# Performance work log

Hardware: AMD Instinct MI355X
Metric: run time of the kernel (lower is better)

The kernel has to match this reference:

```python
import jax, jax.numpy as jnp
import numpy as np

B, L, D, K = 8, 256, 256, 64  # batch, slots, n_input, attn_dimension


def setup_inputs() -> dict:
    key = jax.random.key(0)
    k1, k2, k3 = jax.random.split(key, 3)
    inputs = jax.random.normal(k1, (B, L, D), dtype=jnp.float32)
    # torch.nn.Linear weights are [out_features, in_features]; scale to avoid tanh saturation
    W1 = jax.random.normal(k2, (K, 2 * D), dtype=jnp.float32) * (1.0 / np.sqrt(2 * D))
    W2 = jax.random.normal(k3, (1, K), dtype=jnp.float32) * (1.0 / np.sqrt(K))
    return {"inputs": inputs, "W1": W1, "W2": W2}


def reference(inputs, W1, W2):
    # CONCAT branch of SlotAttention:
    #   score[b,i,j] = W2 @ tanh(W1 @ concat(inputs[b,i], inputs[b,j]))
    # Split W1 into the halves acting on the i-part and j-part of the concat
    # (identical math, avoids materializing the [B,L,L,2D] concat tensor).
    d = inputs.shape[-1]
    W1i, W1j = W1[:, :d], W1[:, d:]
    qi = jnp.einsum('bld,kd->blk', inputs, W1i)          # [B,L,K]
    kj = jnp.einsum('bld,kd->blk', inputs, W1j)          # [B,L,K]
    h = jnp.tanh(qi[:, :, None, :] + kj[:, None, :, :])  # [B,L,L,K]
    scores = jnp.einsum('bijk,k->bij', h, W2[0])         # [B,L,L]
    attn = jax.nn.softmax(scores, axis=2)                # softmax over j
    context = jnp.einsum('bij,bjd->bid', attn, inputs)   # [B,L,D]
    return jnp.concatenate([inputs, context], axis=2)    # [B,L,2D]
```

## Files before the change

### kernel.cpp

```cpp
#include <hip/hip_runtime.h>


#define Bn 8
#define Ln 256
#define Dn 256
#define Kn 64
#define ROWS (Bn*Ln)
#define IPB 4

__global__ __launch_bounds__(128) void proj_kernel(
    const float* __restrict__ X,
    const float* __restrict__ W1,
    float* __restrict__ QK)
{
    __shared__ float Xs[8 * 256];
    const int tid = threadIdx.x;
    const int r0 = blockIdx.x * 8;

    const float4* Xg4 = (const float4*)(X + r0 * Dn);
    float4* Xs4 = (float4*)Xs;
    #pragma unroll
    for (int idx = tid; idx < 512; idx += 128) Xs4[idx] = Xg4[idx];
    __syncthreads();

    const int k = tid & 63, half = tid >> 6;
    const float4* Wrow = (const float4*)(W1 + k * (2 * Dn) + half * Dn);
    float acc[8] = {0, 0, 0, 0, 0, 0, 0, 0};
    #pragma unroll 8
    for (int d4 = 0; d4 < 64; ++d4) {
        float4 w = Wrow[d4];
        #pragma unroll
        for (int r = 0; r < 8; ++r) {
            float4 x = ((const float4*)(Xs + r * Dn))[d4];
            float a = acc[r];
            a = fmaf(w.x, x.x, a);
            a = fmaf(w.y, x.y, a);
            a = fmaf(w.z, x.z, a);
            a = fmaf(w.w, x.w, a);
            acc[r] = a;
        }
    }
    #pragma unroll
    for (int r = 0; r < 8; ++r) {
        float e = __expf(2.0f * acc[r]);
        float t = 1.0f - 2.0f / (e + 1.0f);
        t = fminf(0.99999988f, fmaxf(-0.99999988f, t));
        QK[(r0 + r) * 128 + tid] = t;
    }
}

__global__ __launch_bounds__(256) void attn_kernel(
    const float* __restrict__ X,
    const float* __restrict__ QK,
    const float* __restrict__ W2,
    float* __restrict__ out)
{
    __shared__ float tq_s[IPB * Kn];
    __shared__ float w2_s[Kn];
    __shared__ float S[Ln * IPB];

    const int tid = threadIdx.x;
    const int b  = blockIdx.x / (Ln / IPB);
    const int i0 = (blockIdx.x % (Ln / IPB)) * IPB;

    if (tid < Kn) w2_s[tid] = W2[tid];
    {
        int ii = tid >> 6, kk = tid & 63;
        tq_s[ii * Kn + kk] = QK[(b * Ln + i0 + ii) * 128 + kk];
    }

    float tkr[Kn];
    const float4* kj4 = (const float4*)(QK + (b * Ln + tid) * 128 + 64);
    #pragma unroll
    for (int q = 0; q < 16; ++q) {
        float4 v = kj4[q];
        tkr[q * 4 + 0] = v.x; tkr[q * 4 + 1] = v.y;
        tkr[q * 4 + 2] = v.z; tkr[q * 4 + 3] = v.w;
    }
    __syncthreads();

    float s[IPB] = {0, 0, 0, 0};
    const float4* w4  = (const float4*)w2_s;
    const float4* q4a = (const float4*)(tq_s);
    const float4* q4b = (const float4*)(tq_s + Kn);
    const float4* q4c = (const float4*)(tq_s + 2 * Kn);
    const float4* q4d = (const float4*)(tq_s + 3 * Kn);
    #pragma unroll
    for (int k4 = 0; k4 < 16; ++k4) {
        float4 w  = w4[k4];
        float4 q0 = q4a[k4], q1 = q4b[k4], q2 = q4c[k4], q3 = q4d[k4];
        #pragma unroll
        for (int c = 0; c < 4; ++c) {
            float tk = tkr[k4 * 4 + c];
            float wk = (c == 0) ? w.x : (c == 1) ? w.y : (c == 2) ? w.z : w.w;
            float tq0 = (c == 0) ? q0.x : (c == 1) ? q0.y : (c == 2) ? q0.z : q0.w;
            float tq1 = (c == 0) ? q1.x : (c == 1) ? q1.y : (c == 2) ? q1.z : q1.w;
            float tq2 = (c == 0) ? q2.x : (c == 1) ? q2.y : (c == 2) ? q2.z : q2.w;
            float tq3 = (c == 0) ? q3.x : (c == 1) ? q3.y : (c == 2) ? q3.z : q3.w;
            float n0 = tq0 + tk, d0 = fmaf(tq0, tk, 1.0f);
            float n1 = tq1 + tk, d1 = fmaf(tq1, tk, 1.0f);
            float n2 = tq2 + tk, d2 = fmaf(tq2, tk, 1.0f);
            float n3 = tq3 + tk, d3 = fmaf(tq3, tk, 1.0f);
            s[0] = fmaf(wk, n0 * __builtin_amdgcn_rcpf(d0), s[0]);
            s[1] = fmaf(wk, n1 * __builtin_amdgcn_rcpf(d1), s[1]);
            s[2] = fmaf(wk, n2 * __builtin_amdgcn_rcpf(d2), s[2]);
            s[3] = fmaf(wk, n3 * __builtin_amdgcn_rcpf(d3), s[3]);
        }
    }
    ((float4*)S)[tid] = make_float4(s[0], s[1], s[2], s[3]);
    __syncthreads();

    {
        const int wv = tid >> 6, lane = tid & 63;
        float v0 = S[(lane      ) * IPB + wv];
        float v1 = S[(lane +  64) * IPB + wv];
        float v2 = S[(lane + 128) * IPB + wv];
        float v3 = S[(lane + 192) * IPB + wv];
        float m = fmaxf(fmaxf(v0, v1), fmaxf(v2, v3));
        #pragma unroll
        for (int off = 32; off > 0; off >>= 1)
            m = fmaxf(m, __shfl_xor(m, off));
        float e0 = __expf(v0 - m), e1 = __expf(v1 - m);
        float e2 = __expf(v2 - m), e3 = __expf(v3 - m);
        float sum = e0 + e1 + e2 + e3;
        #pragma unroll
        for (int off = 32; off > 0; off >>= 1)
            sum += __shfl_xor(sum, off);
        float inv = 1.0f / sum;
        S[(lane      ) * IPB + wv] = e0 * inv;
        S[(lane +  64) * IPB + wv] = e1 * inv;
        S[(lane + 128) * IPB + wv] = e2 * inv;
        S[(lane + 192) * IPB + wv] = e3 * inv;
    }
    __syncthreads();

    float a0 = 0, a1 = 0, a2 = 0, a3 = 0;
    const float* Xb = X + b * Ln * Dn;
    const float4* S4 = (const float4*)S;
    #pragma unroll 4
    for (int j = 0; j < Ln; ++j) {
        float4 at = S4[j];
        float x = Xb[j * Dn + tid];
        a0 = fmaf(at.x, x, a0);
        a1 = fmaf(at.y, x, a1);
        a2 = fmaf(at.z, x, a2);
        a3 = fmaf(at.w, x, a3);
    }
    {
        int row = b * Ln + i0;
        out[(row + 0) * (2 * Dn) + tid]      = X[(row + 0) * Dn + tid];
        out[(row + 1) * (2 * Dn) + tid]      = X[(row + 1) * Dn + tid];
        out[(row + 2) * (2 * Dn) + tid]      = X[(row + 2) * Dn + tid];
        out[(row + 3) * (2 * Dn) + tid]      = X[(row + 3) * Dn + tid];
        out[(row + 0) * (2 * Dn) + Dn + tid] = a0;
        out[(row + 1) * (2 * Dn) + Dn + tid] = a1;
        out[(row + 2) * (2 * Dn) + Dn + tid] = a2;
        out[(row + 3) * (2 * Dn) + Dn + tid] = a3;
    }
}

extern "C" void kernel_launch(void* const* d_in, const int* in_sizes, int n_in,
                              void* d_out, int out_size, void* d_ws, size_t ws_size,
                              hipStream_t stream) {
    const float* X  = (const float*)d_in[0];
    const float* W1 = (const float*)d_in[1];
    const float* W2 = (const float*)d_in[2];
    float* out = (float*)d_out;
    float* QK  = (float*)d_ws;

    proj_kernel<<<ROWS / 8, 128, 0, stream>>>(X, W1, QK);
    attn_kernel<<<ROWS / IPB, 256, 0, stream>>>(X, QK, W2, out);
}
```

Before: 95.80 us.

## Split context GEMV over j across waves with float4 loads and LDS reduction

Result: faster. 83.21 us (-13.1%).

```diff
diff --git a/kernel.cpp b/kernel.cpp
--- a/kernel.cpp
+++ b/kernel.cpp
@@ -13,24 +13,24 @@
     const float* __restrict__ W1,
     float* __restrict__ QK)
 {
-    __shared__ float Xs[8 * 256];
+    __shared__ float Xs[4 * 256];
     const int tid = threadIdx.x;
-    const int r0 = blockIdx.x * 8;
+    const int r0 = blockIdx.x * 4;
 
     const float4* Xg4 = (const float4*)(X + r0 * Dn);
     float4* Xs4 = (float4*)Xs;
     #pragma unroll
-    for (int idx = tid; idx < 512; idx += 128) Xs4[idx] = Xg4[idx];
+    for (int idx = tid; idx < 256; idx += 128) Xs4[idx] = Xg4[idx];
     __syncthreads();
 
     const int k = tid & 63, half = tid >> 6;
     const float4* Wrow = (const float4*)(W1 + k * (2 * Dn) + half * Dn);
-    float acc[8] = {0, 0, 0, 0, 0, 0, 0, 0};
+    float acc[4] = {0, 0, 0, 0};
     #pragma unroll 8
     for (int d4 = 0; d4 < 64; ++d4) {
         float4 w = Wrow[d4];
         #pragma unroll
-        for (int r = 0; r < 8; ++r) {
+        for (int r = 0; r < 4; ++r) {
             float4 x = ((const float4*)(Xs + r * Dn))[d4];
             float a = acc[r];
             a = fmaf(w.x, x.x, a);
@@ -41,7 +41,7 @@
         }
     }
     #pragma unroll
-    for (int r = 0; r < 8; ++r) {
+    for (int r = 0; r < 4; ++r) {
         float e = __expf(2.0f * acc[r]);
         float t = 1.0f - 2.0f / (e + 1.0f);
         t = fminf(0.99999988f, fmaxf(-0.99999988f, t));
@@ -58,6 +58,7 @@
     __shared__ float tq_s[IPB * Kn];
     __shared__ float w2_s[Kn];
     __shared__ float S[Ln * IPB];
+    __shared__ float4 red[4 * IPB * 64];
 
     const int tid = threadIdx.x;
     const int b  = blockIdx.x / (Ln / IPB);
@@ -134,28 +135,48 @@
     }
     __syncthreads();
 
-    float a0 = 0, a1 = 0, a2 = 0, a3 = 0;
-    const float* Xb = X + b * Ln * Dn;
-    const float4* S4 = (const float4*)S;
-    #pragma unroll 4
-    for (int j = 0; j < Ln; ++j) {
-        float4 at = S4[j];
-        float x = Xb[j * Dn + tid];
-        a0 = fmaf(at.x, x, a0);
-        a1 = fmaf(at.y, x, a1);
-        a2 = fmaf(at.z, x, a2);
-        a3 = fmaf(at.w, x, a3);
+    {
+        const int wv = tid >> 6, lane = tid & 63;
+        float4 acc0 = {0,0,0,0}, acc1 = {0,0,0,0}, acc2 = {0,0,0,0}, acc3 = {0,0,0,0};
+        const float4* Xb4 = (const float4*)(X + b * Ln * Dn);
+        const float4* S4  = (const float4*)S;
+        const int jbase = wv * 64;
+        #pragma unroll 8
+        for (int jj = 0; jj < 64; ++jj) {
+            int j = jbase + jj;
+            float4 at = S4[j];
+            float4 x  = Xb4[j * 64 + lane];
+            acc0.x = fmaf(at.x, x.x, acc0.x); acc0.y = fmaf(at.x, x.y, acc0.y);
+            acc0.z = fmaf(at.x, x.z, acc0.z); acc0.w = fmaf(at.x, x.w, acc0.w);
+            acc1.x = fmaf(at.y, x.x, acc1.x); acc1.y = fmaf(at.y, x.y, acc1.y);
+            acc1.z = fmaf(at.y, x.z, acc1.z); acc1.w = fmaf(at.y, x.w, acc1.w);
+            acc2.x = fmaf(at.z, x.x, acc2.x); acc2.y = fmaf(at.z, x.y, acc2.y);
+            acc2.z = fmaf(at.z, x.z, acc2.z); acc2.w = fmaf(at.z, x.w, acc2.w);
+            acc3.x = fmaf(at.w, x.x, acc3.x); acc3.y = fmaf(at.w, x.y, acc3.y);
+            acc3.z = fmaf(at.w, x.z, acc3.z); acc3.w = fmaf(at.w, x.w, acc3.w);
+        }
+        red[(wv * IPB + 0) * 64 + lane] = acc0;
+        red[(wv * IPB + 1) * 64 + lane] = acc1;
+        red[(wv * IPB + 2) * 64 + lane] = acc2;
+        red[(wv * IPB + 3) * 64 + lane] = acc3;
     }
+    __syncthreads();
+
     {
-        int row = b * Ln + i0;
-        out[(row + 0) * (2 * Dn) + tid]      = X[(row + 0) * Dn + tid];
-        out[(row + 1) * (2 * Dn) + tid]      = X[(row + 1) * Dn + tid];
-        out[(row + 2) * (2 * Dn) + tid]      = X[(row + 2) * Dn + tid];
-        out[(row + 3) * (2 * Dn) + tid]      = X[(row + 3) * Dn + tid];
-        out[(row + 0) * (2 * Dn) + Dn + tid] = a0;
-        out[(row + 1) * (2 * Dn) + Dn + tid] = a1;
-        out[(row + 2) * (2 * Dn) + Dn + tid] = a2;
-        out[(row + 3) * (2 * Dn) + Dn + tid] = a3;
+        const int i = tid >> 6, q = tid & 63;
+        float4 p0 = red[(0 * IPB + i) * 64 + q];
+        float4 p1 = red[(1 * IPB + i) * 64 + q];
+        float4 p2 = red[(2 * IPB + i) * 64 + q];
+        float4 p3 = red[(3 * IPB + i) * 64 + q];
+        float4 c;
+        c.x = (p0.x + p1.x) + (p2.x + p3.x);
+        c.y = (p0.y + p1.y) + (p2.y + p3.y);
+        c.z = (p0.z + p1.z) + (p2.z + p3.z);
+        c.w = (p0.w + p1.w) + (p2.w + p3.w);
+        const int row = b * Ln + i0 + i;
+        float4 xcopy = ((const float4*)(X + row * Dn))[q];
+        ((float4*)(out + row * 2 * Dn))[q]      = xcopy;
+        ((float4*)(out + row * 2 * Dn + Dn))[q] = c;
     }
 }
 
@@ -168,6 +189,6 @@
     float* out = (float*)d_out;
     float* QK  = (float*)d_ws;
 
-    proj_kernel<<<ROWS / 8, 128, 0, stream>>>(X, W1, QK);
+    proj_kernel<<<ROWS / 4, 128, 0, stream>>>(X, W1, QK);
     attn_kernel<<<ROWS / IPB, 256, 0, stream>>>(X, QK, W2, out);
 }
```
